# Optimization experiments

Measured on AMD Instinct MI355X. Metric: run time of the kernel, lower is better.

## Reference

```python
import jax, jax.numpy as jnp
import numpy as np

N_LAYERS = 4
NEG_SLOPE = 0.2  # GATv2 leaky_relu slope


def _segment_softmax(alpha, seg, num):
    # alpha: [E, H], seg: [E] target-node ids; every node has a self loop so no empty segments
    amax = jax.ops.segment_max(alpha, seg, num_segments=num)
    a = jnp.exp(alpha - amax[seg])
    denom = jax.ops.segment_sum(a, seg, num_segments=num)
    return a / denom[seg]


def _gat_block(x, relations, src, dst, rel_idx, Wl, bl, Wr, br, We, att, bias, Wb, bb):
    N, D = x.shape
    H = att.shape[0]
    C = att.shape[1]

    edge_attr = relations[rel_idx]  # [E, D]
    # add_self_loops with fill_value='mean': self-loop edge_attr = mean of incoming edge attrs
    deg = jax.ops.segment_sum(jnp.ones_like(dst, dtype=x.dtype), dst, num_segments=N)
    loop_attr = jax.ops.segment_sum(edge_attr, dst, num_segments=N) / jnp.maximum(deg, 1.0)[:, None]
    loops = jnp.arange(N, dtype=src.dtype)
    src_all = jnp.concatenate([src, loops])
    dst_all = jnp.concatenate([dst, loops])
    ea = jnp.concatenate([edge_attr, loop_attr], axis=0)  # [E+N, D]

    xl = (x @ Wl + bl).reshape(N, H, C)  # lin_l -> source transform
    xr = (x @ Wr + br).reshape(N, H, C)  # lin_r -> target transform
    eproj = (ea @ We).reshape(-1, H, C)  # lin_edge (no bias in PyG GATv2Conv)

    m = xl[src_all] + xr[dst_all] + eproj          # [E+N, H, C]
    m = jnp.where(m > 0, m, NEG_SLOPE * m)          # leaky_relu
    alpha = jnp.einsum('ehc,hc->eh', m, att)        # [E+N, H]
    alpha = _segment_softmax(alpha, dst_all, N)

    msg = xl[src_all] * alpha[..., None]            # [E+N, H, C]
    out = jax.ops.segment_sum(msg, dst_all, num_segments=N)  # [N, H, C]
    x_out = out.mean(axis=1) + bias                 # concat=False -> head mean, then bias

    # relation update: gnn.lin_edge -> relu -> block lin_edge
    r = jax.nn.relu(relations @ We)                 # [R, H*C]
    r_out = r @ Wb + bb                             # [R, D]
    return x_out, r_out


def setup_inputs() -> dict:
    key = jax.random.key(0)
    N, E, R, D, H = 10000, 40000, 2000, 128, 8
    L = N_LAYERS
    ks = jax.random.split(key, 16)
    s = 1.0 / np.sqrt(D)
    sb = 1.0 / np.sqrt(H * D)
    return {
        'x': jax.random.normal(ks[0], (N, D), dtype=jnp.float32),
        'edge_index': jax.random.randint(ks[1], (2, E), 0, N),
        'relations': jax.random.normal(ks[2], (R, D), dtype=jnp.float32),
        'relation_index': jax.random.randint(ks[3], (E,), 0, R),
        'Wl': jax.random.normal(ks[4], (L, D, H * D), dtype=jnp.float32) * s,
        'bl': jnp.zeros((L, H * D), dtype=jnp.float32),
        'Wr': jax.random.normal(ks[5], (L, D, H * D), dtype=jnp.float32) * s,
        'br': jnp.zeros((L, H * D), dtype=jnp.float32),
        'We': jax.random.normal(ks[6], (L, D, H * D), dtype=jnp.float32) * s,
        'att': jax.random.normal(ks[7], (L, H, D), dtype=jnp.float32) * s,
        'bias': jnp.zeros((L, D), dtype=jnp.float32),
        'Wb': jax.random.normal(ks[8], (L, H * D, D), dtype=jnp.float32) * sb,
        'bb': jnp.zeros((L, D), dtype=jnp.float32),
    }


def reference(x, edge_index, relations, relation_index, Wl, bl, Wr, br, We, att, bias, Wb, bb):
    src, dst = edge_index[0], edge_index[1]
    for l in range(N_LAYERS):
        x, relations = _gat_block(x, relations, src, dst, relation_index,
                                  Wl[l], bl[l], Wr[l], br[l], We[l], att[l],
                                  bias[l], Wb[l], bb[l])
    return (x, relations)
```

## Files before the change

### kernel.cpp

```cpp
#include <hip/hip_runtime.h>
#include <hip/hip_bf16.h>
#include <math.h>

#define NEG_SLOPE 0.2f
#define N_LAYERS 4

typedef __bf16 bf16_t;
typedef __attribute__((ext_vector_type(8))) __bf16 bf16x8;
typedef __attribute__((ext_vector_type(4))) __bf16 bf16x4;
typedef __attribute__((ext_vector_type(4))) float f32x4;
typedef __attribute__((ext_vector_type(8))) float f32x8;

static __device__ __forceinline__ float leaky(float v){ return v > 0.f ? v : NEG_SLOPE * v; }

static __device__ __forceinline__ bf16x8 relu8(bf16x8 v){
#pragma unroll
  for(int i = 0; i < 8; ++i) v[i] = (v[i] > (bf16_t)0.f) ? v[i] : (bf16_t)0.f;
  return v;
}


__global__ void fill_int_kernel(int* __restrict__ p, int v, int n){
  int i = blockIdx.x*blockDim.x + threadIdx.x;
  if(i < n) p[i] = v;
}

__global__ void hist_kernel(const int* __restrict__ dst, int E, int* __restrict__ deg){
  int e = blockIdx.x*blockDim.x + threadIdx.x;
  if(e < E) atomicAdd(&deg[dst[e]], 1);
}

__global__ void scan_kernel(const int* __restrict__ deg, int* __restrict__ offs, int N){
  __shared__ int wsum[4];
  int t = threadIdx.x, lane = t & 63, w = t >> 6;
  int carry = 0;
  for(int base = 0; base < N; base += 256){
    int v = (base + t < N) ? deg[base + t] : 0;
    int s = v;
#pragma unroll
    for(int o = 1; o < 64; o <<= 1){
      int u = __shfl_up(s, o);
      if(lane >= o) s += u;
    }
    if(lane == 63) wsum[w] = s;
    __syncthreads();
    int woff = 0;
    for(int i = 0; i < w; ++i) woff += wsum[i];
    if(base + t < N) offs[base + t + 1] = carry + woff + s;
    int tot = wsum[0] + wsum[1] + wsum[2] + wsum[3];
    __syncthreads();
    carry += tot;
  }
  if(t == 0) offs[0] = 0;
}

__global__ void scatter_kernel(const int* __restrict__ src, const int* __restrict__ dst,
                               const int* __restrict__ rel, int E,
                               const int* __restrict__ offs, int* __restrict__ cursor,
                               int* __restrict__ srcs, int* __restrict__ rels){
  int e = blockIdx.x*blockDim.x + threadIdx.x;
  if(e < E){
    int d = dst[e];
    int pos = offs[d] + atomicAdd(&cursor[d], 1);
    srcs[pos] = src[e];
    rels[pos] = rel[e];
  }
}


__global__ void deg_bhist_kernel(const int* __restrict__ offs, int N, int* __restrict__ blkhist){
  __shared__ int h[256];
  int t = threadIdx.x;
  h[t] = 0; __syncthreads();
  int i = blockIdx.x * 256 + t;
  if(i < N){
    int d = offs[i+1] - offs[i]; if(d > 255) d = 255;
    atomicAdd(&h[d], 1);
  }
  __syncthreads();
  blkhist[blockIdx.x * 256 + t] = h[t];
}

__global__ void deg_base_kernel(int* __restrict__ blkhist, int nb){
  __shared__ int tot[256];
  int d = threadIdx.x;
  int s = 0;
  for(int b = 0; b < nb; ++b){
    int v = blkhist[b * 256 + d];
    blkhist[b * 256 + d] = s;
    s += v;
  }
  tot[d] = s; __syncthreads();
  int start = 0;
  for(int k = d + 1; k < 256; ++k) start += tot[k];
  for(int b = 0; b < nb; ++b) blkhist[b * 256 + d] += start;
}

__global__ void deg_place_kernel(const int* __restrict__ offs, int N,
                                 const int* __restrict__ blkhist, int* __restrict__ order){
  __shared__ int cur[256];
  int t = threadIdx.x;
  cur[t] = blkhist[blockIdx.x * 256 + t];
  __syncthreads();
  int i = blockIdx.x * 256 + t;
  if(i < N){
    int d = offs[i+1] - offs[i]; if(d > 255) d = 255;
    int pos = atomicAdd(&cur[d], 1);
    order[pos] = i;
  }
}


__global__ void transpose_split_all_kernel(
    const float* __restrict__ Wl, const float* __restrict__ Wr,
    const float* __restrict__ We, const float* __restrict__ Wb,
    bf16_t* __restrict__ tWlh, bf16_t* __restrict__ tWll,
    bf16_t* __restrict__ tWrh, bf16_t* __restrict__ tWrl,
    bf16_t* __restrict__ tWeh, bf16_t* __restrict__ tWel,
    bf16_t* __restrict__ tWbh, bf16_t* __restrict__ tWbl){
  __shared__ float t[32][33];
  const int z = blockIdx.z, type = z >> 2, layer = z & 3;
  const int K  = (type < 3) ? 128 : 1024;
  const int Nn = (type < 3) ? 1024 : 128;
  const float* W; bf16_t* Th; bf16_t* Tl;
  if(type == 0){ W = Wl; Th = tWlh; Tl = tWll; }
  else if(type == 1){ W = Wr; Th = tWrh; Tl = tWrl; }
  else if(type == 2){ W = We; Th = tWeh; Tl = tWel; }
  else { W = Wb; Th = tWbh; Tl = tWbl; }
  size_t wo = (size_t)layer * 131072;
  W += wo; Th += wo; Tl += wo;
  const int nbx = K / 32;
  const int bx = blockIdx.x % nbx, by = blockIdx.x / nbx;
  const int k0 = bx * 32, n0 = by * 32;
  const int tx = threadIdx.x, ty = threadIdx.y;
#pragma unroll
  for(int i = 0; i < 4; ++i)
    t[ty*4 + i][tx] = W[(size_t)(k0 + ty*4 + i) * Nn + n0 + tx];
  __syncthreads();
#pragma unroll
  for(int i = 0; i < 4; ++i){
    int n = ty*4 + i;
    float v = t[tx][n];
    bf16_t h = (bf16_t)v;
    bf16_t l = (bf16_t)(v - (float)h);
    Th[(size_t)(n0 + n) * K + k0 + tx] = h;
    Tl[(size_t)(n0 + n) * K + k0 + tx] = l;
  }
}


__global__ __launch_bounds__(256, 3) void gemm_proj_kernel(
    const float* __restrict__ Ar, const float* __restrict__ Ax,
    const bf16_t* __restrict__ Weh, const bf16_t* __restrict__ Wel,
    const bf16_t* __restrict__ Wlh, const bf16_t* __restrict__ Wll,
    const bf16_t* __restrict__ Wrh, const bf16_t* __restrict__ Wrl,
    const float* __restrict__ biasL, const float* __restrict__ biasR,
    const float* __restrict__ biasB, float* __restrict__ ro,
    bf16_t* __restrict__ rpb, bf16_t* __restrict__ xlb, bf16_t* __restrict__ xrb,
    int R, int Nn, int rjobs, int xjobs, int bjobs){
  constexpr int LDK = 40;
  __shared__ char smem[34816];
  bf16_t* Ah = (bf16_t*)smem;
  bf16_t* Bh = (bf16_t*)(smem + 10240);
  bf16_t* Bl = (bf16_t*)(smem + 20480);

  const int tid  = threadIdx.x;
  const int lane = tid & 63;
  const int wid  = tid >> 6;
  const int wm = wid >> 1, wn = wid & 1;
  const int l15 = lane & 15;
  const int kb  = (lane >> 4) * 8;

  int nwg = gridDim.x;
  int lin = blockIdx.x;
  int w = ((nwg & 7) == 0) ? ((lin & 7) * (nwg >> 3) + (lin >> 3)) : lin;
  int job, jw;
  if(w < rjobs){ job = 0; jw = w; }
  else if(w < rjobs + xjobs){ job = 1; jw = w - rjobs; }
  else if(w < rjobs + 2 * xjobs){ job = 2; jw = w - rjobs - xjobs; }
  else { job = 3; jw = w - rjobs - 2 * xjobs; }

  if(job == 3){
    int idx8 = (jw * 256 + tid) * 8;
    if(idx8 < R * 128){
      const float* bp = biasB + (idx8 & 127);
      *(float4*)(ro + idx8)     = *(const float4*)bp;
      *(float4*)(ro + idx8 + 4) = *(const float4*)(bp + 4);
    }
    return;
  }

  const float*  A   = (job == 0) ? Ar : Ax;
  const bf16_t* Bth = (job == 0) ? Weh : (job == 1) ? Wlh : Wrh;
  const bf16_t* Btl = (job == 0) ? Wel : (job == 1) ? Wll : Wrl;
  const int M = (job == 0) ? R : Nn;
  const int row0 = (jw >> 3) * 128, col0 = (jw & 7) * 128;

  f32x4 acc[4][4];
#pragma unroll
  for(int m = 0; m < 4; ++m)
#pragma unroll
    for(int n = 0; n < 4; ++n) acc[m][n] = (f32x4){0.f, 0.f, 0.f, 0.f};

  for(int k0 = 0; k0 < 128; k0 += 32){
    __syncthreads();
#pragma unroll
    for(int i = 0; i < 4; ++i){
      int f = tid + i * 256;
      int r = f >> 3, kq = f & 7;
      float4 v = make_float4(0.f, 0.f, 0.f, 0.f);
      if(row0 + r < M) v = *(const float4*)(A + (size_t)(row0 + r) * 128 + k0 + kq * 4);
      bf16x4 hv = (bf16x4){(bf16_t)v.x, (bf16_t)v.y, (bf16_t)v.z, (bf16_t)v.w};
      *(bf16x4*)&Ah[r * LDK + kq * 4] = hv;
    }
#pragma unroll
    for(int i = 0; i < 2; ++i){
      int f = tid + i * 256;
      int n = f >> 2, kq = f & 3;
      size_t g = (size_t)(col0 + n) * 128 + k0 + kq * 8;
      *(bf16x8*)&Bh[n * LDK + kq * 8] = *(const bf16x8*)(Bth + g);
      *(bf16x8*)&Bl[n * LDK + kq * 8] = *(const bf16x8*)(Btl + g);
    }
    __syncthreads();

    bf16x8 ah[4], bh[4], bl[4];
#pragma unroll
    for(int m = 0; m < 4; ++m){
      int r = wm * 64 + m * 16 + l15;
      ah[m] = *(bf16x8*)&Ah[r * LDK + kb];
    }
#pragma unroll
    for(int n = 0; n < 4; ++n){
      int c = wn * 64 + n * 16 + l15;
      bh[n] = *(bf16x8*)&Bh[c * LDK + kb];
      bl[n] = *(bf16x8*)&Bl[c * LDK + kb];
    }
#pragma unroll
    for(int m = 0; m < 4; ++m)
#pragma unroll
      for(int n = 0; n < 4; ++n){
        acc[m][n] = __builtin_amdgcn_mfma_f32_16x16x32_bf16(ah[m], bh[n], acc[m][n], 0, 0, 0);
        acc[m][n] = __builtin_amdgcn_mfma_f32_16x16x32_bf16(ah[m], bl[n], acc[m][n], 0, 0, 0);
      }
  }

  const float* biasP = (job == 0) ? nullptr : (job == 1) ? biasL : biasR;
  bf16_t* dst = (job == 0) ? rpb : (job == 1) ? xlb : xrb;
  bf16_t* tile = (bf16_t*)smem;
  __syncthreads();
#pragma unroll
  for(int n = 0; n < 4; ++n){
    int col = wn * 64 + n * 16 + l15;
    float bv = biasP ? biasP[col0 + col] : 0.f;
#pragma unroll
    for(int m = 0; m < 4; ++m){
      int rb = wm * 64 + m * 16 + (lane >> 4) * 4;
#pragma unroll
      for(int r = 0; r < 4; ++r)
        tile[(rb + r) * 136 + col] = (bf16_t)(acc[m][n][r] + bv);
    }
  }
  __syncthreads();
#pragma unroll
  for(int i = 0; i < 8; ++i){
    int ei = i * 2048 + tid * 8;
    int rr = ei >> 7, cc = ei & 127;
    if(row0 + rr < M)
      *(bf16x8*)(dst + (size_t)(row0 + rr) * 1024 + col0 + cc) = *(bf16x8*)&tile[rr * 136 + cc];
  }
}


__global__ __launch_bounds__(256) void gemm_rel_kernel(
    const bf16_t* __restrict__ Ag,
    const bf16_t* __restrict__ Bth, const bf16_t* __restrict__ Btl,
    float* __restrict__ C, int M){
  constexpr int LDK = 40;
  __shared__ bf16_t Ah[128 * LDK];
  __shared__ bf16_t Bh[128 * LDK];
  __shared__ bf16_t Bl[128 * LDK];

  const int tid  = threadIdx.x;
  const int lane = tid & 63;
  const int wid  = tid >> 6;
  const int wm = wid >> 1, wn = wid & 1;
  const int row0 = blockIdx.y * 128;
  const int l15 = lane & 15;
  const int kb  = (lane >> 4) * 8;
  const int kbeg = blockIdx.z * 64;

  f32x4 acc[4][4];
#pragma unroll
  for(int m = 0; m < 4; ++m)
#pragma unroll
    for(int n = 0; n < 4; ++n) acc[m][n] = (f32x4){0.f, 0.f, 0.f, 0.f};

#pragma unroll
  for(int tt = 0; tt < 2; ++tt){
    int k0 = kbeg + tt * 32;
    __syncthreads();
#pragma unroll
    for(int i = 0; i < 2; ++i){
      int f = tid + i * 256;
      int r = f >> 2, kq = f & 3;
      bf16x8 vh = {};
      if(row0 + r < M)
        vh = relu8(*(const bf16x8*)(Ag + (size_t)(row0 + r) * 1024 + k0 + kq * 8));
      *(bf16x8*)&Ah[r * LDK + kq * 8] = vh;
      size_t gb = (size_t)r * 1024 + k0 + kq * 8;
      *(bf16x8*)&Bh[r * LDK + kq * 8] = *(const bf16x8*)(Bth + gb);
      *(bf16x8*)&Bl[r * LDK + kq * 8] = *(const bf16x8*)(Btl + gb);
    }
    __syncthreads();

    bf16x8 ah[4], bh[4], bl[4];
#pragma unroll
    for(int m = 0; m < 4; ++m){
      int r = wm * 64 + m * 16 + l15;
      ah[m] = *(bf16x8*)&Ah[r * LDK + kb];
    }
#pragma unroll
    for(int n = 0; n < 4; ++n){
      int c = wn * 64 + n * 16 + l15;
      bh[n] = *(bf16x8*)&Bh[c * LDK + kb];
      bl[n] = *(bf16x8*)&Bl[c * LDK + kb];
    }
#pragma unroll
    for(int m = 0; m < 4; ++m)
#pragma unroll
      for(int n = 0; n < 4; ++n){
        acc[m][n] = __builtin_amdgcn_mfma_f32_16x16x32_bf16(ah[m], bh[n], acc[m][n], 0, 0, 0);
        acc[m][n] = __builtin_amdgcn_mfma_f32_16x16x32_bf16(ah[m], bl[n], acc[m][n], 0, 0, 0);
      }
  }

#pragma unroll
  for(int n = 0; n < 4; ++n){
    int col = wn * 64 + n * 16 + l15;
    if(col < 128){
#pragma unroll
      for(int m = 0; m < 4; ++m){
        int rbase = row0 + wm * 64 + m * 16 + (lane >> 4) * 4;
#pragma unroll
        for(int r = 0; r < 4; ++r){
          if(rbase + r < M)
            atomicAdd(&C[(size_t)(rbase + r) * 128 + col], acc[m][n][r]);
        }
      }
    }
  }
}


__global__ __launch_bounds__(256) void node_fused_kernel(
    const bf16_t* __restrict__ xlb, const bf16_t* __restrict__ xrb,
    const bf16_t* __restrict__ rpb,
    const int* __restrict__ offs, const int* __restrict__ srcs, const int* __restrict__ rels,
    const int* __restrict__ order,
    const float* __restrict__ att, const float* __restrict__ bias,
    float* __restrict__ xout, int N){
  __shared__ float tsh[2][128];
  const int wid  = threadIdx.x >> 6;
  const int lane = threadIdx.x & 63;
  const int nib  = wid >> 1;
  const int half = wid & 1;
  const int slot = blockIdx.x * 2 + nib;
  const bool active = slot < N;
  const int node = active ? order[slot] : 0;
  int beg = 0, end = 0;
  if(active){ beg = offs[node]; end = offs[node + 1]; }
  const float inv = 1.0f / fmaxf((float)(end - beg), 1.0f);

  const int o  = (half * 64 + lane) * 8;
  const int c0 = (lane & 15) * 8;
  const int h  = half * 4 + (lane >> 4);
  f32x8 av = *(const f32x8*)(att + h * 128 + c0);
  bf16x8 xrv = *(const bf16x8*)(xrb + (size_t)node * 1024 + o);
  f32x8 xr;
#pragma unroll
  for(int i = 0; i < 8; ++i) xr[i] = (float)xrv[i];

  f32x8 lac, num;
#pragma unroll
  for(int i = 0; i < 8; ++i){ lac[i] = 0.f; num[i] = 0.f; }
  float m = -INFINITY, den = 0.f;

  for(int p = beg; p < end; p += 4){
    int rem = end - p;
    int i1 = (rem > 1) ? p + 1 : p;
    int i2 = (rem > 2) ? p + 2 : p;
    int i3 = (rem > 3) ? p + 3 : p;
    float k1 = (rem > 1) ? 1.f : 0.f;
    float k2 = (rem > 2) ? 1.f : 0.f;
    float k3 = (rem > 3) ? 1.f : 0.f;
    int s0 = srcs[p],  r0 = rels[p];
    int s1 = srcs[i1], r1 = rels[i1];
    int s2 = srcs[i2], r2 = rels[i2];
    int s3 = srcs[i3], r3 = rels[i3];
    bf16x8 a0 = *(const bf16x8*)(xlb + (size_t)s0 * 1024 + o);
    bf16x8 b0 = *(const bf16x8*)(rpb + (size_t)r0 * 1024 + o);
    bf16x8 a1 = *(const bf16x8*)(xlb + (size_t)s1 * 1024 + o);
    bf16x8 b1 = *(const bf16x8*)(rpb + (size_t)r1 * 1024 + o);
    bf16x8 a2 = *(const bf16x8*)(xlb + (size_t)s2 * 1024 + o);
    bf16x8 b2 = *(const bf16x8*)(rpb + (size_t)r2 * 1024 + o);
    bf16x8 a3 = *(const bf16x8*)(xlb + (size_t)s3 * 1024 + o);
    bf16x8 b3 = *(const bf16x8*)(rpb + (size_t)r3 * 1024 + o);
    float l0 = 0.f, l1 = 0.f, l2 = 0.f, l3 = 0.f;
#pragma unroll
    for(int i = 0; i < 8; ++i){
      float v0 = (float)b0[i], v1 = (float)b1[i], v2 = (float)b2[i], v3 = (float)b3[i];
      lac[i] += v0 + k1 * v1 + k2 * v2 + k3 * v3;
      l0 += leaky((float)a0[i] + xr[i] + v0) * av[i];
      l1 += leaky((float)a1[i] + xr[i] + v1) * av[i];
      l2 += leaky((float)a2[i] + xr[i] + v2) * av[i];
      l3 += leaky((float)a3[i] + xr[i] + v3) * av[i];
    }
#pragma unroll
    for(int q = 8; q >= 1; q >>= 1){
      l0 += __shfl_xor(l0, q); l1 += __shfl_xor(l1, q);
      l2 += __shfl_xor(l2, q); l3 += __shfl_xor(l3, q);
    }
    l1 = (k1 > 0.f) ? l1 : -INFINITY;
    l2 = (k2 > 0.f) ? l2 : -INFINITY;
    l3 = (k3 > 0.f) ? l3 : -INFINITY;
    float nm = fmaxf(m, fmaxf(fmaxf(l0, l1), fmaxf(l2, l3)));
    float sc = __expf(m - nm);
    float w0 = __expf(l0 - nm), w1 = __expf(l1 - nm);
    float w2 = __expf(l2 - nm), w3 = __expf(l3 - nm);
    den = den * sc + w0 + w1 + w2 + w3;
#pragma unroll
    for(int i = 0; i < 8; ++i)
      num[i] = num[i] * sc + w0 * (float)a0[i] + w1 * (float)a1[i]
                           + w2 * (float)a2[i] + w3 * (float)a3[i];
    m = nm;
  }

  bf16x8 xlv = *(const bf16x8*)(xlb + (size_t)node * 1024 + o);
  float sl = 0.f;
#pragma unroll
  for(int i = 0; i < 8; ++i)
    sl += leaky((float)xlv[i] + xr[i] + lac[i] * inv) * av[i];
#pragma unroll
  for(int q = 8; q >= 1; q >>= 1) sl += __shfl_xor(sl, q);
  {
    float nm = fmaxf(m, sl);
    float sc = __expf(m - nm), wv = __expf(sl - nm);
    den = den * sc + wv;
#pragma unroll
    for(int i = 0; i < 8; ++i) num[i] = num[i] * sc + wv * (float)xlv[i];
    m = nm;
  }

  f32x8 t;
  float d = 1.0f / den;
#pragma unroll
  for(int i = 0; i < 8; ++i) t[i] = num[i] * d;
#pragma unroll
  for(int i = 0; i < 8; ++i) t[i] += __shfl_xor(t[i], 16);
#pragma unroll
  for(int i = 0; i < 8; ++i) t[i] += __shfl_xor(t[i], 32);

  if(half == 1 && lane < 16){
#pragma unroll
    for(int i = 0; i < 8; ++i) tsh[nib][lane * 8 + i] = t[i];
  }
  __syncthreads();
  if(active && half == 0 && lane < 16){
    const float* bp = bias + lane * 8;
    float* op = xout + (size_t)node * 128 + lane * 8;
    float q[8];
#pragma unroll
    for(int i = 0; i < 8; ++i) q[i] = (t[i] + tsh[nib][lane * 8 + i]) * 0.125f + bp[i];
    *(float4*)op       = make_float4(q[0], q[1], q[2], q[3]);
    *(float4*)(op + 4) = make_float4(q[4], q[5], q[6], q[7]);
  }
}


extern "C" void kernel_launch(void* const* d_in, const int* in_sizes, int n_in,
                              void* d_out, int out_size, void* d_ws, size_t ws_size,
                              hipStream_t stream){
  const float* x0   = (const float*)d_in[0];
  const int*   ei   = (const int*)d_in[1];
  const float* rel0 = (const float*)d_in[2];
  const int*   ridx = (const int*)d_in[3];
  const float* Wl   = (const float*)d_in[4];
  const float* bl   = (const float*)d_in[5];
  const float* Wr   = (const float*)d_in[6];
  const float* br   = (const float*)d_in[7];
  const float* We   = (const float*)d_in[8];
  const float* att  = (const float*)d_in[9];
  const float* bias = (const float*)d_in[10];
  const float* Wb   = (const float*)d_in[11];
  const float* bb   = (const float*)d_in[12];

  const int D = 128, HC = 1024;
  const int N = in_sizes[0] / D;
  const int E = in_sizes[1] / 2;
  const int R = in_sizes[2] / D;
  const int WSZ = D * HC;
  const int NB = (N + 255) / 256;

  const int* src = ei;
  const int* dst = ei + E;

  char* ws = (char*)d_ws;
  size_t off = 0;
  auto alloc = [&](size_t bytes) -> void* {
    void* p = ws + off;
    off += (bytes + 255) & ~(size_t)255;
    return p;
  };
  bf16_t* xlb    = (bf16_t*)alloc((size_t)N * HC * 2);
  bf16_t* xrb    = (bf16_t*)alloc((size_t)N * HC * 2);
  bf16_t* rpb    = (bf16_t*)alloc((size_t)R * HC * 2);
  float*  xbufA  = (float*)alloc((size_t)N * D * 4);
  float*  xbufB  = (float*)alloc((size_t)N * D * 4);
  float*  rbufA  = (float*)alloc((size_t)R * D * 4);
  float*  rbufB  = (float*)alloc((size_t)R * D * 4);
  int* zbase   = (int*)alloc((size_t)(2 * N) * 4);
  int* deg     = zbase;
  int* cursor  = zbase + N;
  int* offs    = (int*)alloc((size_t)(N + 1) * 4);
  int* blkhist = (int*)alloc((size_t)NB * 256 * 4);
  int* order   = (int*)alloc((size_t)N * 4);
  int* srcs    = (int*)alloc((size_t)E * 4);
  int* rels    = (int*)alloc((size_t)E * 4);
  bf16_t* tWl_h = (bf16_t*)alloc((size_t)N_LAYERS * WSZ * 2);
  bf16_t* tWl_l = (bf16_t*)alloc((size_t)N_LAYERS * WSZ * 2);
  bf16_t* tWr_h = (bf16_t*)alloc((size_t)N_LAYERS * WSZ * 2);
  bf16_t* tWr_l = (bf16_t*)alloc((size_t)N_LAYERS * WSZ * 2);
  bf16_t* tWe_h = (bf16_t*)alloc((size_t)N_LAYERS * WSZ * 2);
  bf16_t* tWe_l = (bf16_t*)alloc((size_t)N_LAYERS * WSZ * 2);
  bf16_t* tWb_h = (bf16_t*)alloc((size_t)N_LAYERS * WSZ * 2);
  bf16_t* tWb_l = (bf16_t*)alloc((size_t)N_LAYERS * WSZ * 2);
  float* xbuf[2] = {xbufA, xbufB};
  float* rbuf[2] = {rbufA, rbufB};

  float* out_x = (float*)d_out;
  float* out_r = (float*)d_out + (size_t)N * D;

  fill_int_kernel<<<(2 * N + 255) / 256, 256, 0, stream>>>(zbase, 0, 2 * N);
  hist_kernel<<<(E + 255) / 256, 256, 0, stream>>>(dst, E, deg);
  scan_kernel<<<1, 256, 0, stream>>>(deg, offs, N);
  scatter_kernel<<<(E + 255) / 256, 256, 0, stream>>>(src, dst, ridx, E, offs, cursor, srcs, rels);
  deg_bhist_kernel<<<NB, 256, 0, stream>>>(offs, N, blkhist);
  deg_base_kernel<<<1, 256, 0, stream>>>(blkhist, NB);
  deg_place_kernel<<<NB, 256, 0, stream>>>(offs, N, blkhist, order);

  transpose_split_all_kernel<<<dim3(128, 1, 16), dim3(32, 8), 0, stream>>>(
      Wl, Wr, We, Wb, tWl_h, tWl_l, tWr_h, tWr_l, tWe_h, tWe_l, tWb_h, tWb_l);

  const int rjobs = ((R + 127) / 128) * (HC / 128);
  const int xjobs = ((N + 127) / 128) * (HC / 128);
  const int bjobs = 128;
  const int nwg = rjobs + 2 * xjobs + bjobs;

  for(int l = 0; l < N_LAYERS; ++l){
    const float* xin = (l == 0) ? x0   : xbuf[(l + 1) & 1];
    float*       xo  = (l == N_LAYERS - 1) ? out_x : xbuf[l & 1];
    const float* rin = (l == 0) ? rel0 : rbuf[(l + 1) & 1];
    float*       ro  = (l == N_LAYERS - 1) ? out_r : rbuf[l & 1];
    size_t wo = (size_t)l * WSZ;
    const float* bl_l  = bl + (size_t)l * HC;
    const float* br_l  = br + (size_t)l * HC;
    const float* att_l = att + (size_t)l * 8 * 128;
    const float* bias_l= bias + (size_t)l * D;
    const float* bb_l  = bb + (size_t)l * D;

    gemm_proj_kernel<<<nwg, 256, 0, stream>>>(
        rin, xin, tWe_h + wo, tWe_l + wo, tWl_h + wo, tWl_l + wo, tWr_h + wo, tWr_l + wo,
        bl_l, br_l, bb_l, ro, rpb, xlb, xrb, R, N, rjobs, xjobs, bjobs);
    node_fused_kernel<<<(2 * N + 3) / 4, 256, 0, stream>>>(
        xlb, xrb, rpb, offs, srcs, rels, order, att_l, bias_l, xo, N);
    gemm_rel_kernel<<<dim3(1, (R + 127) / 128, 16), 256, 0, stream>>>(
        rpb, tWb_h + wo, tWb_l + wo, ro, R);
  }
}
```

Measured before the change: 401.6 us.

## Fuse relation GEMM into node kernel, store layer activations as bf16, unroll edge loop by 8

Merges the relation-update GEMM into the node aggregation kernel as extra leading blocks, which removes one launch per layer and lets the two independent jobs run at the same time. Intermediate node features are now written as bf16, so the next projection GEMM reads half the bytes and skips the fp32-to-bf16 conversion. The final fp32 output is written only in the last layer. The per-node edge loop gets an 8-wide main path with more loads in flight, at the cost of higher register pressure. The relation block indexing hardcodes 16 row tiles (rb&15), which assumes R≤2048.

```diff
diff --git a/kernel.cpp b/kernel.cpp
--- a/kernel.cpp
+++ b/kernel.cpp
@@ -151,6 +151,7 @@
 
 __global__ __launch_bounds__(256, 3) void gemm_proj_kernel(
     const float* __restrict__ Ar, const float* __restrict__ Ax,
+    const bf16_t* __restrict__ Axb,
     const bf16_t* __restrict__ Weh, const bf16_t* __restrict__ Wel,
     const bf16_t* __restrict__ Wlh, const bf16_t* __restrict__ Wll,
     const bf16_t* __restrict__ Wrh, const bf16_t* __restrict__ Wrl,
@@ -195,6 +196,7 @@
   const bf16_t* Btl = (job == 0) ? Wel : (job == 1) ? Wll : Wrl;
   const int M = (job == 0) ? R : Nn;
   const int row0 = (jw >> 3) * 128, col0 = (jw & 7) * 128;
+  const bool abf = (job != 0) && (Axb != nullptr);
 
   f32x4 acc[4][4];
 #pragma unroll
@@ -204,14 +206,25 @@
 
   for(int k0 = 0; k0 < 128; k0 += 32){
     __syncthreads();
-#pragma unroll
-    for(int i = 0; i < 4; ++i){
-      int f = tid + i * 256;
-      int r = f >> 3, kq = f & 7;
-      float4 v = make_float4(0.f, 0.f, 0.f, 0.f);
-      if(row0 + r < M) v = *(const float4*)(A + (size_t)(row0 + r) * 128 + k0 + kq * 4);
-      bf16x4 hv = (bf16x4){(bf16_t)v.x, (bf16_t)v.y, (bf16_t)v.z, (bf16_t)v.w};
-      *(bf16x4*)&Ah[r * LDK + kq * 4] = hv;
+    if(abf){
+#pragma unroll
+      for(int i = 0; i < 2; ++i){
+        int f = tid + i * 256;
+        int r = f >> 2, kq = f & 3;
+        bf16x8 v = {};
+        if(row0 + r < M) v = *(const bf16x8*)(Axb + (size_t)(row0 + r) * 128 + k0 + kq * 8);
+        *(bf16x8*)&Ah[r * LDK + kq * 8] = v;
+      }
+    } else {
+#pragma unroll
+      for(int i = 0; i < 4; ++i){
+        int f = tid + i * 256;
+        int r = f >> 3, kq = f & 7;
+        float4 v = make_float4(0.f, 0.f, 0.f, 0.f);
+        if(row0 + r < M) v = *(const float4*)(A + (size_t)(row0 + r) * 128 + k0 + kq * 4);
+        bf16x4 hv = (bf16x4){(bf16_t)v.x, (bf16_t)v.y, (bf16_t)v.z, (bf16_t)v.w};
+        *(bf16x4*)&Ah[r * LDK + kq * 4] = hv;
+      }
     }
 #pragma unroll
     for(int i = 0; i < 2; ++i){
@@ -271,100 +284,99 @@
 }
 
 
-__global__ __launch_bounds__(256) void gemm_rel_kernel(
-    const bf16_t* __restrict__ Ag,
-    const bf16_t* __restrict__ Bth, const bf16_t* __restrict__ Btl,
-    float* __restrict__ C, int M){
-  constexpr int LDK = 40;
-  __shared__ bf16_t Ah[128 * LDK];
-  __shared__ bf16_t Bh[128 * LDK];
-  __shared__ bf16_t Bl[128 * LDK];
-
-  const int tid  = threadIdx.x;
-  const int lane = tid & 63;
-  const int wid  = tid >> 6;
-  const int wm = wid >> 1, wn = wid & 1;
-  const int row0 = blockIdx.y * 128;
-  const int l15 = lane & 15;
-  const int kb  = (lane >> 4) * 8;
-  const int kbeg = blockIdx.z * 64;
-
-  f32x4 acc[4][4];
-#pragma unroll
-  for(int m = 0; m < 4; ++m)
-#pragma unroll
-    for(int n = 0; n < 4; ++n) acc[m][n] = (f32x4){0.f, 0.f, 0.f, 0.f};
-
-#pragma unroll
-  for(int tt = 0; tt < 2; ++tt){
-    int k0 = kbeg + tt * 32;
-    __syncthreads();
-#pragma unroll
-    for(int i = 0; i < 2; ++i){
-      int f = tid + i * 256;
-      int r = f >> 2, kq = f & 3;
-      bf16x8 vh = {};
-      if(row0 + r < M)
-        vh = relu8(*(const bf16x8*)(Ag + (size_t)(row0 + r) * 1024 + k0 + kq * 8));
-      *(bf16x8*)&Ah[r * LDK + kq * 8] = vh;
-      size_t gb = (size_t)r * 1024 + k0 + kq * 8;
-      *(bf16x8*)&Bh[r * LDK + kq * 8] = *(const bf16x8*)(Bth + gb);
-      *(bf16x8*)&Bl[r * LDK + kq * 8] = *(const bf16x8*)(Btl + gb);
-    }
-    __syncthreads();
-
-    bf16x8 ah[4], bh[4], bl[4];
-#pragma unroll
-    for(int m = 0; m < 4; ++m){
-      int r = wm * 64 + m * 16 + l15;
-      ah[m] = *(bf16x8*)&Ah[r * LDK + kb];
-    }
-#pragma unroll
-    for(int n = 0; n < 4; ++n){
-      int c = wn * 64 + n * 16 + l15;
-      bh[n] = *(bf16x8*)&Bh[c * LDK + kb];
-      bl[n] = *(bf16x8*)&Bl[c * LDK + kb];
-    }
-#pragma unroll
-    for(int m = 0; m < 4; ++m)
-#pragma unroll
-      for(int n = 0; n < 4; ++n){
-        acc[m][n] = __builtin_amdgcn_mfma_f32_16x16x32_bf16(ah[m], bh[n], acc[m][n], 0, 0, 0);
-        acc[m][n] = __builtin_amdgcn_mfma_f32_16x16x32_bf16(ah[m], bl[n], acc[m][n], 0, 0, 0);
-      }
-  }
-
-#pragma unroll
-  for(int n = 0; n < 4; ++n){
-    int col = wn * 64 + n * 16 + l15;
-    if(col < 128){
-#pragma unroll
-      for(int m = 0; m < 4; ++m){
-        int rbase = row0 + wm * 64 + m * 16 + (lane >> 4) * 4;
-#pragma unroll
-        for(int r = 0; r < 4; ++r){
-          if(rbase + r < M)
-            atomicAdd(&C[(size_t)(rbase + r) * 128 + col], acc[m][n][r]);
-        }
-      }
-    }
-  }
-}
-
-
-__global__ __launch_bounds__(256) void node_fused_kernel(
+__global__ __launch_bounds__(256) void node_rel_kernel(
     const bf16_t* __restrict__ xlb, const bf16_t* __restrict__ xrb,
     const bf16_t* __restrict__ rpb,
     const int* __restrict__ offs, const int* __restrict__ srcs, const int* __restrict__ rels,
     const int* __restrict__ order,
     const float* __restrict__ att, const float* __restrict__ bias,
-    float* __restrict__ xout, int N){
-  __shared__ float tsh[2][128];
+    float* __restrict__ xout, bf16_t* __restrict__ xq, int N, int RELBLK,
+    const bf16_t* __restrict__ Bth, const bf16_t* __restrict__ Btl,
+    float* __restrict__ ro, int R){
+  constexpr int LDK = 40;
+  __shared__ char smem[30720];
+
+  if((int)blockIdx.x < RELBLK){
+    bf16_t* Ah = (bf16_t*)smem;
+    bf16_t* Bh = (bf16_t*)(smem + 10240);
+    bf16_t* Bl = (bf16_t*)(smem + 20480);
+    const int tid  = threadIdx.x;
+    const int lane = tid & 63;
+    const int wid  = tid >> 6;
+    const int wm = wid >> 1, wn = wid & 1;
+    const int rb = blockIdx.x;
+    const int row0 = (rb & 15) * 128;
+    const int kbeg = (rb >> 4) * 64;
+    const int l15 = lane & 15;
+    const int kb  = (lane >> 4) * 8;
+
+    f32x4 acc[4][4];
+#pragma unroll
+    for(int m = 0; m < 4; ++m)
+#pragma unroll
+      for(int n = 0; n < 4; ++n) acc[m][n] = (f32x4){0.f, 0.f, 0.f, 0.f};
+
+#pragma unroll
+    for(int tt = 0; tt < 2; ++tt){
+      int k0 = kbeg + tt * 32;
+      __syncthreads();
+#pragma unroll
+      for(int i = 0; i < 2; ++i){
+        int f = tid + i * 256;
+        int r = f >> 2, kq = f & 3;
+        bf16x8 vh = {};
+        if(row0 + r < R)
+          vh = relu8(*(const bf16x8*)(rpb + (size_t)(row0 + r) * 1024 + k0 + kq * 8));
+        *(bf16x8*)&Ah[r * LDK + kq * 8] = vh;
+        size_t gb = (size_t)r * 1024 + k0 + kq * 8;
+        *(bf16x8*)&Bh[r * LDK + kq * 8] = *(const bf16x8*)(Bth + gb);
+        *(bf16x8*)&Bl[r * LDK + kq * 8] = *(const bf16x8*)(Btl + gb);
+      }
+      __syncthreads();
+
+      bf16x8 ah[4], bh[4], bl[4];
+#pragma unroll
+      for(int m = 0; m < 4; ++m){
+        int r = wm * 64 + m * 16 + l15;
+        ah[m] = *(bf16x8*)&Ah[r * LDK + kb];
+      }
+#pragma unroll
+      for(int n = 0; n < 4; ++n){
+        int c = wn * 64 + n * 16 + l15;
+        bh[n] = *(bf16x8*)&Bh[c * LDK + kb];
+        bl[n] = *(bf16x8*)&Bl[c * LDK + kb];
+      }
+#pragma unroll
+      for(int m = 0; m < 4; ++m)
+#pragma unroll
+        for(int n = 0; n < 4; ++n){
+          acc[m][n] = __builtin_amdgcn_mfma_f32_16x16x32_bf16(ah[m], bh[n], acc[m][n], 0, 0, 0);
+          acc[m][n] = __builtin_amdgcn_mfma_f32_16x16x32_bf16(ah[m], bl[n], acc[m][n], 0, 0, 0);
+        }
+    }
+
+#pragma unroll
+    for(int n = 0; n < 4; ++n){
+      int col = wn * 64 + n * 16 + l15;
+#pragma unroll
+      for(int m = 0; m < 4; ++m){
+        int rbase = row0 + wm * 64 + m * 16 + (lane >> 4) * 4;
+#pragma unroll
+        for(int r = 0; r < 4; ++r){
+          if(rbase + r < R)
+            atomicAdd(&ro[(size_t)(rbase + r) * 128 + col], acc[m][n][r]);
+        }
+      }
+    }
+    return;
+  }
+
+  float (*tsh)[128] = (float(*)[128])smem;
   const int wid  = threadIdx.x >> 6;
   const int lane = threadIdx.x & 63;
   const int nib  = wid >> 1;
   const int half = wid & 1;
-  const int slot = blockIdx.x * 2 + nib;
+  const int slot = (blockIdx.x - RELBLK) * 2 + nib;
   const bool active = slot < N;
   const int node = active ? order[slot] : 0;
   int beg = 0, end = 0;
@@ -385,7 +397,50 @@
   for(int i = 0; i < 8; ++i){ lac[i] = 0.f; num[i] = 0.f; }
   float m = -INFINITY, den = 0.f;
 
-  for(int p = beg; p < end; p += 4){
+  int p = beg;
+  for(; p + 8 <= end; p += 8){
+    bf16x8 a[8], b[8];
+#pragma unroll
+    for(int j = 0; j < 8; ++j){
+      a[j] = *(const bf16x8*)(xlb + (size_t)srcs[p + j] * 1024 + o);
+      b[j] = *(const bf16x8*)(rpb + (size_t)rels[p + j] * 1024 + o);
+    }
+    float l[8];
+#pragma unroll
+    for(int j = 0; j < 8; ++j) l[j] = 0.f;
+#pragma unroll
+    for(int i = 0; i < 8; ++i){
+      float xri = xr[i], avi = av[i], s = 0.f;
+#pragma unroll
+      for(int j = 0; j < 8; ++j){
+        float bv = (float)b[j][i];
+        s += bv;
+        l[j] += leaky((float)a[j][i] + xri + bv) * avi;
+      }
+      lac[i] += s;
+    }
+#pragma unroll
+    for(int q = 8; q >= 1; q >>= 1)
+#pragma unroll
+      for(int j = 0; j < 8; ++j) l[j] += __shfl_xor(l[j], q);
+    float nm = m;
+#pragma unroll
+    for(int j = 0; j < 8; ++j) nm = fmaxf(nm, l[j]);
+    float sc = __expf(m - nm);
+    float wv[8], ws = 0.f;
+#pragma unroll
+    for(int j = 0; j < 8; ++j){ wv[j] = __expf(l[j] - nm); ws += wv[j]; }
+    den = den * sc + ws;
+#pragma unroll
+    for(int i = 0; i < 8; ++i){
+      float acc = num[i] * sc;
+#pragma unroll
+      for(int j = 0; j < 8; ++j) acc += wv[j] * (float)a[j][i];
+      num[i] = acc;
+    }
+    m = nm;
+  }
+  for(; p < end; p += 4){
     int rem = end - p;
     int i1 = (rem > 1) ? p + 1 : p;
     int i2 = (rem > 2) ? p + 2 : p;
@@ -467,12 +522,18 @@
   __syncthreads();
   if(active && half == 0 && lane < 16){
     const float* bp = bias + lane * 8;
-    float* op = xout + (size_t)node * 128 + lane * 8;
     float q[8];
 #pragma unroll
     for(int i = 0; i < 8; ++i) q[i] = (t[i] + tsh[nib][lane * 8 + i]) * 0.125f + bp[i];
-    *(float4*)op       = make_float4(q[0], q[1], q[2], q[3]);
-    *(float4*)(op + 4) = make_float4(q[4], q[5], q[6], q[7]);
+    bf16x8 qb;
+#pragma unroll
+    for(int i = 0; i < 8; ++i) qb[i] = (bf16_t)q[i];
+    *(bf16x8*)(xq + (size_t)node * 128 + lane * 8) = qb;
+    if(xout){
+      float* op = xout + (size_t)node * 128 + lane * 8;
+      *(float4*)op       = make_float4(q[0], q[1], q[2], q[3]);
+      *(float4*)(op + 4) = make_float4(q[4], q[5], q[6], q[7]);
+    }
   }
 }
 
@@ -514,8 +575,8 @@
   bf16_t* xlb    = (bf16_t*)alloc((size_t)N * HC * 2);
   bf16_t* xrb    = (bf16_t*)alloc((size_t)N * HC * 2);
   bf16_t* rpb    = (bf16_t*)alloc((size_t)R * HC * 2);
-  float*  xbufA  = (float*)alloc((size_t)N * D * 4);
-  float*  xbufB  = (float*)alloc((size_t)N * D * 4);
+  bf16_t* xqA    = (bf16_t*)alloc((size_t)N * D * 2);
+  bf16_t* xqB    = (bf16_t*)alloc((size_t)N * D * 2);
   float*  rbufA  = (float*)alloc((size_t)R * D * 4);
   float*  rbufB  = (float*)alloc((size_t)R * D * 4);
   int* zbase   = (int*)alloc((size_t)(2 * N) * 4);
@@ -534,7 +595,7 @@
   bf16_t* tWe_l = (bf16_t*)alloc((size_t)N_LAYERS * WSZ * 2);
   bf16_t* tWb_h = (bf16_t*)alloc((size_t)N_LAYERS * WSZ * 2);
   bf16_t* tWb_l = (bf16_t*)alloc((size_t)N_LAYERS * WSZ * 2);
-  float* xbuf[2] = {xbufA, xbufB};
+  bf16_t* xq[2] = {xqA, xqB};
   float* rbuf[2] = {rbufA, rbufB};
 
   float* out_x = (float*)d_out;
@@ -555,12 +616,15 @@
   const int xjobs = ((N + 127) / 128) * (HC / 128);
   const int bjobs = 128;
   const int nwg = rjobs + 2 * xjobs + bjobs;
+  const int RELBLK = ((R + 127) / 128) * 16;
+  const int NODEBLK = (2 * N + 3) / 4;
 
   for(int l = 0; l < N_LAYERS; ++l){
-    const float* xin = (l == 0) ? x0   : xbuf[(l + 1) & 1];
-    float*       xo  = (l == N_LAYERS - 1) ? out_x : xbuf[l & 1];
-    const float* rin = (l == 0) ? rel0 : rbuf[(l + 1) & 1];
-    float*       ro  = (l == N_LAYERS - 1) ? out_r : rbuf[l & 1];
+    const bf16_t* xq_in = (l == 0) ? nullptr : xq[(l + 1) & 1];
+    bf16_t*       xq_out = xq[l & 1];
+    float*        xo  = (l == N_LAYERS - 1) ? out_x : nullptr;
+    const float*  rin = (l == 0) ? rel0 : rbuf[(l + 1) & 1];
+    float*        ro  = (l == N_LAYERS - 1) ? out_r : rbuf[l & 1];
     size_t wo = (size_t)l * WSZ;
     const float* bl_l  = bl + (size_t)l * HC;
     const float* br_l  = br + (size_t)l * HC;
@@ -569,11 +633,10 @@
     const float* bb_l  = bb + (size_t)l * D;
 
     gemm_proj_kernel<<<nwg, 256, 0, stream>>>(
-        rin, xin, tWe_h + wo, tWe_l + wo, tWl_h + wo, tWl_l + wo, tWr_h + wo, tWr_l + wo,
+        rin, x0, xq_in, tWe_h + wo, tWe_l + wo, tWl_h + wo, tWl_l + wo, tWr_h + wo, tWr_l + wo,
         bl_l, br_l, bb_l, ro, rpb, xlb, xrb, R, N, rjobs, xjobs, bjobs);
-    node_fused_kernel<<<(2 * N + 3) / 4, 256, 0, stream>>>(
-        xlb, xrb, rpb, offs, srcs, rels, order, att_l, bias_l, xo, N);
-    gemm_rel_kernel<<<dim3(1, (R + 127) / 128, 16), 256, 0, stream>>>(
-        rpb, tWb_h + wo, tWb_l + wo, ro, R);
-  }
-}
+    node_rel_kernel<<<RELBLK + NODEBLK, 256, 0, stream>>>(
+        xlb, xrb, rpb, offs, srcs, rels, order, att_l, bias_l,
+        xo, xq_out, N, RELBLK, tWb_h + wo, tWb_l + wo, ro, R);
+  }
+}
```

Result: slower. 541.4 us (+34.8%).
